# Kernel optimization log

Hardware: AMD Instinct MI355X
Metric: run time of the kernel (lower is better)

The kernel has to match this reference:

```python
import jax, jax.numpy as jnp
import numpy as np

H, C = 16, 5           # GAT heads, per-head out channels
SIZE = 500             # max_pool_x size (time bins)
GAT_SLOPE, ACT_SLOPE = 0.2, 0.01


def _lrelu(x, s):
    return jnp.where(x >= 0, x, s * x)


def _gat(x, src, dst, ea, mask, W, We, a_s, a_d, a_e, b):
    # PyG GATConv: shared src/dst lin, edge_dim, self-loops already appended by caller
    N = x.shape[0]
    xp = (x @ W.T).reshape(N, H, C)                                   # [N,H,C]
    al = (jnp.einsum('nhc,hc->nh', xp, a_s)[src]
          + jnp.einsum('nhc,hc->nh', xp, a_d)[dst]
          + jnp.einsum('ehc,hc->eh', (ea @ We.T).reshape(-1, H, C), a_e))  # [E,H]
    al = _lrelu(al, GAT_SLOPE)
    if mask is not None:  # masked-out edges contribute nothing (equivalent to edge removal)
        al = jnp.where(mask[:, None], al, -jnp.inf)
    m = jax.ops.segment_max(al, dst, num_segments=N)                  # finite: every node has a self-loop
    e = jnp.exp(al - m[dst])
    coef = e / jax.ops.segment_sum(e, dst, num_segments=N)[dst]       # segment softmax over incoming edges
    out = jax.ops.segment_sum(coef[:, :, None] * xp[src], dst, num_segments=N)
    return out.reshape(N, H * C) + b


def _conv(x, w, b):
    y = jax.lax.conv_general_dilated(x, w, (2,), [(1, 1)],
                                     dimension_numbers=('NCH', 'OIH', 'NCH'))
    return y + b[None, :, None]


def _mlp(z, w1, b1, w2, b2, w3, b3):
    z = _lrelu(z @ w1.T + b1, ACT_SLOPE)
    z = _lrelu(z @ w2.T + b2, ACT_SLOPE)
    return z @ w3.T + b3


def _forward(x, edge_attr,
             gat1_W, gat1_We, gat1_as, gat1_ad, gat1_ae, gat1_b,
             gat2_W, gat2_We, gat2_as, gat2_ad, gat2_ae, gat2_b,
             conv1_w, conv1_b, conv2_w, conv2_b, conv3_w, conv3_b,
             chi_w1, chi_b1, chi_w2, chi_b2, chi_w3, chi_b3,
             rp_w1, rp_b1, rp_w2, rp_b2, rp_w3, rp_b3,
             t0_w1, t0_b1, t0_w2, t0_b2, t0_w3, t0_b3,
             edge_index, num_graphs):
    N = x.shape[0]
    loops = jnp.arange(N, dtype=edge_index.dtype)
    src = jnp.concatenate([edge_index[0], loops])
    dst = jnp.concatenate([edge_index[1], loops])
    ea = jnp.concatenate([edge_attr, jnp.zeros((N, edge_attr.shape[1]), edge_attr.dtype)], axis=0)
    timing = x[:, 2].astype(jnp.int32)   # non-differentiable, like .to(torch.long)

    h = _gat(x, src, dst, ea, None, gat1_W, gat1_We, gat1_as, gat1_ad, gat1_ae, gat1_b)
    mask2 = jnp.concatenate([edge_attr[:, 0] > 1.0, jnp.ones((N,), bool)])  # EdgeV[:,0]>1 + self loops
    h = _gat(h, src, dst, ea, mask2, gat2_W, gat2_We, gat2_as, gat2_ad, gat2_ae, gat2_b)

    # max_pool_x(cluster=Timing, batch, size=500): scatter-max into B*500 slots,
    # empty slots -> 0 (torch_scatter semantics); then view(-1, 80, 500)
    pooled = jax.ops.segment_max(h, timing, num_segments=num_graphs * SIZE)
    pooled = jnp.where(jnp.isfinite(pooled), pooled, 0.0)
    z = pooled.reshape(num_graphs, H * C, SIZE)

    z = _lrelu(_conv(z, conv1_w, conv1_b), ACT_SLOPE)   # [B,16,247]
    z = _lrelu(_conv(z, conv2_w, conv2_b), ACT_SLOPE)   # [B,16,120]
    z = _lrelu(_conv(z, conv3_w, conv3_b), ACT_SLOPE)   # [B,16,57]
    L = z.shape[-1]
    nw = (L - 10) // 10 + 1                              # MaxPool1d(k=10,s=10) -> 5
    z = z[..., :nw * 10].reshape(z.shape[0], z.shape[1], nw, 10).max(-1)
    z = z.reshape(z.shape[0], -1)                        # [B,80]

    chi0 = jnp.tanh(_mlp(z, chi_w1, chi_b1, chi_w2, chi_b2, chi_w3, chi_b3))
    rp = _mlp(z, rp_w1, rp_b1, rp_w2, rp_b2, rp_w3, rp_b3)
    t0 = _mlp(z, t0_w1, t0_b1, t0_w2, t0_b2, t0_w3, t0_b3)
    return jnp.concatenate([chi0, rp, t0], axis=1)       # [B,3]


def setup_inputs() -> dict:
    key = jax.random.key(0)
    ki = iter(jax.random.split(key, 50))
    N, E, B = 100_000, 1_200_000, 64
    x = jax.random.normal(next(ki), (N, 5), jnp.float32)
    timing = jax.random.randint(next(ki), (N,), 0, SIZE)
    x = x.at[:, 2].set(timing.astype(jnp.float32))       # Timing column holds integer bins
    src = jax.random.randint(next(ki), (E,), 0, N, dtype=jnp.int32)
    off = jax.random.randint(next(ki), (E,), 1, N, dtype=jnp.int32)
    dst = (src + off) % N                                # no pre-existing self-loops (PyG strips them)
    edge_index = jnp.stack([src, dst])
    edge_attr = jax.random.uniform(next(ki), (E, 2), jnp.float32) * 3.0  # ~2/3 pass col0>1 mask
    batch = jnp.sort(jax.random.randint(next(ki), (N,), 0, B, dtype=jnp.int32))

    def p(shape, scale=0.1):
        return jax.random.normal(next(ki), shape, jnp.float32) * scale

    return dict(
        x=x, edge_attr=edge_attr,
        gat1_W=p((80, 5)), gat1_We=p((80, 2)), gat1_as=p((16, 5)), gat1_ad=p((16, 5)), gat1_ae=p((16, 5)), gat1_b=p((80,)),
        gat2_W=p((80, 80)), gat2_We=p((80, 2)), gat2_as=p((16, 5)), gat2_ad=p((16, 5)), gat2_ae=p((16, 5)), gat2_b=p((80,)),
        conv1_w=p((16, 80, 10)), conv1_b=p((16,)),
        conv2_w=p((16, 16, 10)), conv2_b=p((16,)),
        conv3_w=p((16, 16, 10)), conv3_b=p((16,)),
        chi_w1=p((128, 80)), chi_b1=p((128,)), chi_w2=p((128, 128)), chi_b2=p((128,)), chi_w3=p((1, 128)), chi_b3=p((1,)),
        rp_w1=p((128, 80)), rp_b1=p((128,)), rp_w2=p((128, 128)), rp_b2=p((128,)), rp_w3=p((1, 128)), rp_b3=p((1,)),
        t0_w1=p((128, 80)), t0_b1=p((128,)), t0_w2=p((128, 128)), t0_b2=p((128,)), t0_w3=p((1, 128)), t0_b3=p((1,)),
        edge_index=edge_index, batch=batch, num_graphs=B)


def reference(x, edge_attr,
              gat1_W, gat1_We, gat1_as, gat1_ad, gat1_ae, gat1_b,
              gat2_W, gat2_We, gat2_as, gat2_ad, gat2_ae, gat2_b,
              conv1_w, conv1_b, conv2_w, conv2_b, conv3_w, conv3_b,
              chi_w1, chi_b1, chi_w2, chi_b2, chi_w3, chi_b3,
              rp_w1, rp_b1, rp_w2, rp_b2, rp_w3, rp_b3,
              t0_w1, t0_b1, t0_w2, t0_b2, t0_w3, t0_b3,
              edge_index, batch, num_graphs):
    del batch  # only used in torch to compute batch_size (passed here as num_graphs)
    return _forward(x, edge_attr,
                    gat1_W, gat1_We, gat1_as, gat1_ad, gat1_ae, gat1_b,
                    gat2_W, gat2_We, gat2_as, gat2_ad, gat2_ae, gat2_b,
                    conv1_w, conv1_b, conv2_w, conv2_b, conv3_w, conv3_b,
                    chi_w1, chi_b1, chi_w2, chi_b2, chi_w3, chi_b3,
                    rp_w1, rp_b1, rp_w2, rp_b2, rp_w3, rp_b3,
                    t0_w1, t0_b1, t0_w2, t0_b2, t0_w3, t0_b3,
                    edge_index, num_graphs)
```

## Files before the change

kernel.cpp:

```cpp
#include <hip/hip_runtime.h>
#include <math.h>

#define DEV static __device__ __forceinline__

DEV unsigned fenc(float f) {
    unsigned u = __float_as_uint(f);
    return (u & 0x80000000u) ? ~u : (u | 0x80000000u);
}
DEV float fdec(unsigned u) {
    return __uint_as_float((u & 0x80000000u) ? (u ^ 0x80000000u) : ~u);
}
DEV void atomic_max_u32(unsigned* p, unsigned v) {
    __hip_atomic_fetch_max(p, v, __ATOMIC_RELAXED, __HIP_MEMORY_SCOPE_AGENT);
}
DEV unsigned bf16(float f) {
    unsigned u = __float_as_uint(f);
    return (u + 0x7FFFu + ((u >> 16) & 1u)) >> 16;
}
DEV float unbf16(unsigned s) { return __uint_as_float(s << 16); }

__global__ void k_proj5t(const float* __restrict__ x, const float* __restrict__ W,
                         const float* __restrict__ a_s, const float* __restrict__ a_d,
                         unsigned short* __restrict__ xpb, float* __restrict__ dterm, int N) {
    int i = blockIdx.x * blockDim.x + threadIdx.x;
    if (i >= N * 16) return;
    int n = i >> 4, h = i & 15;
    float xr[5];
    #pragma unroll
    for (int j = 0; j < 5; ++j) xr[j] = x[(size_t)n * 5 + j];
    float o[5];
    #pragma unroll
    for (int c = 0; c < 5; ++c) {
        const float* wr = W + (size_t)(h * 5 + c) * 5;
        float s = 0.f;
        #pragma unroll
        for (int j = 0; j < 5; ++j) s += xr[j] * wr[j];
        o[c] = s;
    }
    float ss = 0.f, sd = 0.f;
    #pragma unroll
    for (int c = 0; c < 5; ++c) { ss += o[c] * a_s[h * 5 + c]; sd += o[c] * a_d[h * 5 + c]; }
    unsigned* p = (unsigned*)(xpb + (size_t)n * 96 + h * 6);
    p[0] = bf16(o[0]) | (bf16(o[1]) << 16);
    p[1] = bf16(o[2]) | (bf16(o[3]) << 16);
    p[2] = bf16(o[4]) | (bf16(ss) << 16);
    dterm[i] = sd;
}

__global__ __launch_bounds__(256) void k_proj80t(
    const unsigned short* __restrict__ in,
    const float* __restrict__ W,
    const float* __restrict__ a_s, const float* __restrict__ a_d,
    unsigned short* __restrict__ xpb, float* __restrict__ dterm, int N) {
    __shared__ float XS[16 * 136];
    __shared__ float WS[16 * 81];
    int tid = threadIdx.x;
    int n0 = blockIdx.x * 128;
    int h = tid & 15, ng = tid >> 4;

    float acc[8][5];
    #pragma unroll
    for (int j = 0; j < 8; ++j)
        #pragma unroll
        for (int c = 0; c < 5; ++c) acc[j][c] = 0.f;

    for (int k0 = 0; k0 < 80; k0 += 16) {
        __syncthreads();
        {
            int r = tid >> 1;
            int halfk = (tid & 1) * 8;
            int n = n0 + r; if (n >= N) n = N - 1;
            const uint4 v = *(const uint4*)(in + (size_t)n * 80 + k0 + halfk);
            unsigned uu[4] = {v.x, v.y, v.z, v.w};
            #pragma unroll
            for (int j = 0; j < 4; ++j) {
                XS[(halfk + 2 * j)     * 136 + r] = unbf16(uu[j] & 0xffff);
                XS[(halfk + 2 * j + 1) * 136 + r] = unbf16(uu[j] >> 16);
            }
        }
        {
            #pragma unroll
            for (int i = 0; i < 5; ++i) {
                int j = tid + i * 256;
                int oc = j >> 4, kk = j & 15;
                WS[kk * 81 + oc] = W[(size_t)oc * 80 + k0 + kk];
            }
        }
        __syncthreads();
        #pragma unroll
        for (int kk = 0; kk < 16; ++kk) {
            float4 xa = *(const float4*)&XS[kk * 136 + ng * 8];
            float4 xb = *(const float4*)&XS[kk * 136 + ng * 8 + 4];
            float wv[5];
            #pragma unroll
            for (int c = 0; c < 5; ++c) wv[c] = WS[kk * 81 + h * 5 + c];
            float xv[8] = {xa.x, xa.y, xa.z, xa.w, xb.x, xb.y, xb.z, xb.w};
            #pragma unroll
            for (int j = 0; j < 8; ++j)
                #pragma unroll
                for (int c = 0; c < 5; ++c) acc[j][c] += xv[j] * wv[c];
        }
    }
    float as_[5], ad_[5];
    #pragma unroll
    for (int c = 0; c < 5; ++c) { as_[c] = a_s[h * 5 + c]; ad_[c] = a_d[h * 5 + c]; }
    #pragma unroll
    for (int j = 0; j < 8; ++j) {
        int n = n0 + ng * 8 + j;
        if (n < N) {
            float ss = 0.f, sd = 0.f;
            #pragma unroll
            for (int c = 0; c < 5; ++c) { ss += acc[j][c] * as_[c]; sd += acc[j][c] * ad_[c]; }
            unsigned* p = (unsigned*)(xpb + (size_t)n * 96 + h * 6);
            p[0] = bf16(acc[j][0]) | (bf16(acc[j][1]) << 16);
            p[1] = bf16(acc[j][2]) | (bf16(acc[j][3]) << 16);
            p[2] = bf16(acc[j][4]) | (bf16(ss) << 16);
            dterm[n * 16 + h] = sd;
        }
    }
}

__global__ void k_hist(const int* __restrict__ dst, int* __restrict__ deg, int E) {
    int e4 = (blockIdx.x * blockDim.x + threadIdx.x) * 4;
    if (e4 >= E) return;
    if (e4 + 3 < E) {
        int4 d = *(const int4*)(dst + e4);
        __hip_atomic_fetch_add(&deg[d.x], 1, __ATOMIC_RELAXED, __HIP_MEMORY_SCOPE_AGENT);
        __hip_atomic_fetch_add(&deg[d.y], 1, __ATOMIC_RELAXED, __HIP_MEMORY_SCOPE_AGENT);
        __hip_atomic_fetch_add(&deg[d.z], 1, __ATOMIC_RELAXED, __HIP_MEMORY_SCOPE_AGENT);
        __hip_atomic_fetch_add(&deg[d.w], 1, __ATOMIC_RELAXED, __HIP_MEMORY_SCOPE_AGENT);
    } else {
        for (int e = e4; e < E; ++e)
            __hip_atomic_fetch_add(&deg[dst[e]], 1, __ATOMIC_RELAXED, __HIP_MEMORY_SCOPE_AGENT);
    }
}

#define SCAN_B 256
__global__ void k_bsum(const int* __restrict__ deg, int* __restrict__ bsum, int N) {
    __shared__ int sm[SCAN_B];
    int i = blockIdx.x * SCAN_B + threadIdx.x;
    sm[threadIdx.x] = (i < N) ? deg[i] : 0;
    __syncthreads();
    for (int s = SCAN_B / 2; s > 0; s >>= 1) {
        if (threadIdx.x < s) sm[threadIdx.x] += sm[threadIdx.x + s];
        __syncthreads();
    }
    if (threadIdx.x == 0) bsum[blockIdx.x] = sm[0];
}

__global__ void k_bscan(int* __restrict__ bsum, int G) {
    __shared__ int sm[512];
    int t = threadIdx.x;
    int orig = (t < G) ? bsum[t] : 0;
    sm[t] = orig;
    __syncthreads();
    for (int s = 1; s < 512; s <<= 1) {
        int v = (t >= s) ? sm[t - s] : 0;
        __syncthreads();
        sm[t] += v;
        __syncthreads();
    }
    if (t < G) bsum[t] = sm[t] - orig;
}

__global__ void k_apply(const int* __restrict__ deg, int* __restrict__ off,
                        int* __restrict__ bcur, const int* __restrict__ bsum, int N) {
    __shared__ int sm[SCAN_B];
    int i = blockIdx.x * SCAN_B + threadIdx.x;
    int v = (i < N) ? deg[i] : 0;
    sm[threadIdx.x] = v;
    __syncthreads();
    for (int s = 1; s < SCAN_B; s <<= 1) {
        int t = (threadIdx.x >= s) ? sm[threadIdx.x - s] : 0;
        __syncthreads();
        sm[threadIdx.x] += t;
        __syncthreads();
    }
    if (i < N) {
        int excl = bsum[blockIdx.x] + sm[threadIdx.x] - v;
        off[i] = excl;
        if ((i & 255) == 0) bcur[i >> 8] = excl;
        if (i == N - 1) off[N] = excl + v;
    }
}

#define BIN_TILE 4096
__global__ __launch_bounds__(256) void k_bin(const int* __restrict__ src,
        const int* __restrict__ dst, const float* __restrict__ ea,
        int* __restrict__ bcur, uint4* __restrict__ ebuf, int E, int NB) {
    __shared__ int cnt[512];
    __shared__ int base[512];
    int tid = threadIdx.x;
    for (int b = tid; b < NB; b += 256) cnt[b] = 0;
    __syncthreads();
    int e0 = blockIdx.x * BIN_TILE;
    #pragma unroll
    for (int k = 0; k < BIN_TILE / 256; ++k) {
        int e = e0 + k * 256 + tid;
        if (e < E) atomicAdd(&cnt[((unsigned)dst[e]) >> 8], 1);
    }
    __syncthreads();
    for (int b = tid; b < NB; b += 256) {
        int c = cnt[b];
        base[b] = c ? __hip_atomic_fetch_add(&bcur[b], c, __ATOMIC_RELAXED,
                                             __HIP_MEMORY_SCOPE_AGENT) : 0;
        cnt[b] = 0;
    }
    __syncthreads();
    #pragma unroll
    for (int k = 0; k < BIN_TILE / 256; ++k) {
        int e = e0 + k * 256 + tid;
        if (e < E) {
            int d = dst[e];
            int b = ((unsigned)d) >> 8;
            int r = atomicAdd(&cnt[b], 1);
            float a0 = ea[2 * e], a1 = ea[2 * e + 1];
            unsigned s = (unsigned)src[e] | (a0 > 1.0f ? 0x80000000u : 0u);
            ebuf[base[b] + r] = make_uint4(s, bf16(a0) | (bf16(a1) << 16), (unsigned)d, 0u);
        }
    }
}

__global__ __launch_bounds__(256) void k_perm(const int* __restrict__ off,
        const uint4* __restrict__ ebuf, uint2* __restrict__ erec, int N) {
    __shared__ int cur[256];
    int b = blockIdx.x, tid = threadIdx.x;
    int d0 = b << 8;
    int dEnd = d0 + 256; if (dEnd > N) dEnd = N;
    if (d0 + tid < N) cur[tid] = off[d0 + tid];
    int seg0 = off[d0], seg1 = off[dEnd];
    __syncthreads();
    for (int i = seg0 + tid; i < seg1; i += 256) {
        uint4 r = ebuf[i];
        int p = atomicAdd(&cur[(int)r.z - d0], 1);
        erec[p] = make_uint2(r.x, r.y);
    }
}

template<bool MASKED, bool OUT_BF16>
__global__ void k_gat(const int* __restrict__ off, const uint2* __restrict__ erec,
                      const float* __restrict__ dterm,
                      const float* __restrict__ We, const float* __restrict__ a_e,
                      const unsigned short* __restrict__ xpb,
                      const float* __restrict__ bias, void* __restrict__ hout, int N) {
    int i = blockIdx.x * blockDim.x + threadIdx.x;
    if (i >= N * 16) return;
    int d = i >> 4, h = i & 15;
    float q0 = 0.f, q1 = 0.f;
    #pragma unroll
    for (int c = 0; c < 5; ++c) {
        float ae = a_e[h * 5 + c];
        q0 += We[(h * 5 + c) * 2 + 0] * ae;
        q1 += We[(h * 5 + c) * 2 + 1] * ae;
    }
    float dt = dterm[i];
    int e0 = off[d], e1 = off[d + 1];

    float m, den = 1.f, n0, n1, n2, n3, n4;
    {
        const uint3 v = *(const uint3*)(xpb + (size_t)d * 96 + h * 6);
        n0 = unbf16(v.x & 0xffff); n1 = unbf16(v.x >> 16);
        n2 = unbf16(v.y & 0xffff); n3 = unbf16(v.y >> 16);
        n4 = unbf16(v.z & 0xffff);
        float sl = unbf16(v.z >> 16) + dt;
        m = fmaxf(sl, 0.2f * sl);
    }

    uint2 r_cur = make_uint2(0, 0), r_nxt = make_uint2(0, 0);
    uint3 v_cur = make_uint3(0, 0, 0), v_nxt = make_uint3(0, 0, 0);
    if (e0 < e1) {
        r_cur = erec[e0];
        if (!MASKED || (r_cur.x >> 31))
            v_cur = *(const uint3*)(xpb + (size_t)(r_cur.x & 0x7fffffff) * 96 + h * 6);
    }
    if (e0 + 1 < e1) r_nxt = erec[e0 + 1];
    for (int e = e0; e < e1; ++e) {
        uint2 r_n2 = make_uint2(0, 0);
        if (e + 2 < e1) r_n2 = erec[e + 2];
        if (e + 1 < e1 && (!MASKED || (r_nxt.x >> 31)))
            v_nxt = *(const uint3*)(xpb + (size_t)(r_nxt.x & 0x7fffffff) * 96 + h * 6);
        bool keep = !MASKED || (r_cur.x >> 31);
        if (keep) {
            float ea0 = unbf16(r_cur.y & 0xffff), ea1 = unbf16(r_cur.y >> 16);
            uint3 v = v_cur;
            float st = unbf16(v.z >> 16);
            float al = st + dt + ea0 * q0 + ea1 * q1;
            al = fmaxf(al, 0.2f * al);
            float x0 = unbf16(v.x & 0xffff), x1 = unbf16(v.x >> 16);
            float x2 = unbf16(v.y & 0xffff), x3 = unbf16(v.y >> 16);
            float x4 = unbf16(v.z & 0xffff);
            bool gt = al > m;
            float t = __expf(-fabsf(al - m));
            float c = gt ? t : 1.f;
            float w = gt ? 1.f : t;
            m = fmaxf(m, al);
            den = den * c + w;
            n0 = n0 * c + w * x0;
            n1 = n1 * c + w * x1;
            n2 = n2 * c + w * x2;
            n3 = n3 * c + w * x3;
            n4 = n4 * c + w * x4;
        }
        r_cur = r_nxt; r_nxt = r_n2; v_cur = v_nxt;
    }
    float inv = 1.0f / den;
    const float* br = bias + h * 5;
    float v0 = n0 * inv + br[0];
    float v1 = n1 * inv + br[1];
    float v2 = n2 * inv + br[2];
    float v3 = n3 * inv + br[3];
    float v4 = n4 * inv + br[4];
    if (OUT_BF16) {
        unsigned short* orow = (unsigned short*)hout + (size_t)d * 80 + h * 5;
        orow[0] = (unsigned short)bf16(v0);
        orow[1] = (unsigned short)bf16(v1);
        orow[2] = (unsigned short)bf16(v2);
        orow[3] = (unsigned short)bf16(v3);
        orow[4] = (unsigned short)bf16(v4);
    } else {
        float* orow = (float*)hout + (size_t)d * 80 + h * 5;
        orow[0] = v0; orow[1] = v1; orow[2] = v2; orow[3] = v3; orow[4] = v4;
    }
}

__global__ void k_pool8(const float* __restrict__ x, const float* __restrict__ h2,
                        unsigned* __restrict__ psl, int N) {
    int i = blockIdx.x * blockDim.x + threadIdx.x;
    if (i >= N * 80) return;
    int n = i / 80, ch = i % 80;
    int t = (int)x[(size_t)n * 5 + 2];
    unsigned* slice = psl + (size_t)(blockIdx.x & 7) * 40000;
    atomic_max_u32(&slice[t * 80 + ch], fenc(h2[i]));
}

__global__ void k_poolred(const unsigned* __restrict__ psl, float* __restrict__ pool) {
    int i = blockIdx.x * blockDim.x + threadIdx.x;
    if (i >= 40000) return;
    unsigned m = 0u;
    #pragma unroll
    for (int s = 0; s < 8; ++s) m = max(m, psl[s * 40000 + i]);
    pool[i] = (m == 0u) ? 0.f : fdec(m);
}

__global__ __launch_bounds__(256) void k_conv1(const float* __restrict__ pool,
        const float* __restrict__ w, const float* __restrict__ b,
        float* __restrict__ c1) {
    __shared__ float XS[80 * 44];
    __shared__ float WS[16 * 972];
    int gg = blockIdx.x >> 4, chunk = blockIdx.x & 15;
    int t0 = chunk * 16;
    int tid = threadIdx.x;
    for (int idx = tid; idx < 80 * 44; idx += 256) {
        int ic = idx / 44, j = idx % 44;
        int p = 2 * t0 - 1 + j;
        XS[idx] = (gg == 0 && j < 41 && p >= 0 && p < 500) ? pool[ic * 500 + p] : 0.f;
    }
    for (int idx = tid; idx < 12800; idx += 256) {
        int oc = idx / 800, r = idx % 800;
        int ic = r / 10, k = r % 10;
        WS[oc * 972 + ic * 12 + k] = w[idx];
    }
    __syncthreads();
    int oc = tid >> 4, tg = tid & 15;
    float acc = 0.f;
    for (int ic = 0; ic < 80; ++ic) {
        const float* xr = &XS[ic * 44 + 2 * tg];
        const float* wr = &WS[oc * 972 + ic * 12];
        #pragma unroll
        for (int k = 0; k < 10; ++k) acc += xr[k] * wr[k];
    }
    int t = t0 + tg;
    if (t < 247) {
        float s = acc + b[oc];
        c1[(size_t)gg * 3952 + oc * 247 + t] = s >= 0.f ? s : 0.01f * s;
    }
}

__global__ __launch_bounds__(128) void k_conv2(const float* __restrict__ c1,
        const float* __restrict__ w2c, const float* __restrict__ b2c,
        float* __restrict__ c2g) {
    __shared__ float Z1[16 * 248];
    __shared__ float WS[160];
    int g = blockIdx.x >> 4, oc = blockIdx.x & 15;
    int tid = threadIdx.x;
    for (int idx = tid; idx < 16 * 247; idx += 128) {
        int ic = idx / 247, t = idx % 247;
        Z1[ic * 248 + t] = c1[(size_t)g * 3952 + idx];
    }
    for (int idx = tid; idx < 160; idx += 128) WS[idx] = w2c[oc * 160 + idx];
    __syncthreads();
    if (tid < 120) {
        float s = b2c[oc];
        #pragma unroll 4
        for (int ic = 0; ic < 16; ++ic) {
            const float* xr = &Z1[ic * 248];
            const float* wr = &WS[ic * 10];
            #pragma unroll
            for (int k = 0; k < 10; ++k) {
                int p = 2 * tid + k - 1;
                if (p >= 0 && p < 247) s += xr[p] * wr[k];
            }
        }
        c2g[g * 1920 + oc * 120 + tid] = s >= 0.f ? s : 0.01f * s;
    }
}

__global__ __launch_bounds__(128) void k_conv3(const float* __restrict__ c2g,
        const float* __restrict__ w3c, const float* __restrict__ b3c,
        float* __restrict__ c3g) {
    __shared__ float Z2[16 * 121];
    __shared__ float WS[160];
    int g = blockIdx.x >> 4, oc = blockIdx.x & 15;
    int tid = threadIdx.x;
    for (int idx = tid; idx < 16 * 120; idx += 128) {
        int ic = idx / 120, t = idx % 120;
        Z2[ic * 121 + t] = c2g[g * 1920 + idx];
    }
    for (int idx = tid; idx < 160; idx += 128) WS[idx] = w3c[oc * 160 + idx];
    __syncthreads();
    if (tid < 57) {
        float s = b3c[oc];
        #pragma unroll 4
        for (int ic = 0; ic < 16; ++ic) {
            const float* xr = &Z2[ic * 121];
            const float* wr = &WS[ic * 10];
            #pragma unroll
            for (int k = 0; k < 10; ++k) {
                int p = 2 * tid + k - 1;
                if (p >= 0 && p < 120) s += xr[p] * wr[k];
            }
        }
        c3g[g * 912 + oc * 57 + tid] = s >= 0.f ? s : 0.01f * s;
    }
}

struct HeadW { const float *w1, *b1, *w2, *b2, *w3, *b3; };

__global__ __launch_bounds__(128) void k_heads(const float* __restrict__ c3g,
        HeadW hw0, HeadW hw1, HeadW hw2, float* __restrict__ houts) {
    __shared__ float Z3[16 * 57];
    __shared__ float ZF[80], HB[128], HC[128];
    __shared__ float partial[2];
    int g = blockIdx.x / 3, hd = blockIdx.x % 3;
    int tid = threadIdx.x;
    const HeadW hw = (hd == 0) ? hw0 : (hd == 1) ? hw1 : hw2;
    for (int idx = tid; idx < 912; idx += 128) Z3[idx] = c3g[g * 912 + idx];
    __syncthreads();
    if (tid < 80) {
        int ch = tid / 5, wd = tid % 5;
        const float* p = &Z3[ch * 57 + wd * 10];
        float m = p[0];
        #pragma unroll
        for (int k = 1; k < 10; ++k) m = fmaxf(m, p[k]);
        ZF[tid] = m;
    }
    __syncthreads();
    float s = hw.b1[tid];
    for (int k = 0; k < 80; ++k) s += ZF[k] * hw.w1[tid * 80 + k];
    HB[tid] = s >= 0.f ? s : 0.01f * s;
    __syncthreads();
    s = hw.b2[tid];
    for (int k = 0; k < 128; ++k) s += HB[k] * hw.w2[tid * 128 + k];
    HC[tid] = s >= 0.f ? s : 0.01f * s;
    __syncthreads();
    float p = HC[tid] * hw.w3[tid];
    #pragma unroll
    for (int o = 32; o > 0; o >>= 1) p += __shfl_down(p, o, 64);
    if ((tid & 63) == 0) partial[tid >> 6] = p;
    __syncthreads();
    if (tid == 0) {
        float o = partial[0] + partial[1] + hw.b3[0];
        houts[g * 3 + hd] = (hd == 0) ? tanhf(o) : o;
    }
}

__global__ void k_bcast(const float* __restrict__ houts, float* __restrict__ out, int B3) {
    int i = blockIdx.x * blockDim.x + threadIdx.x;
    if (i >= B3) return;
    out[i] = (i < 3) ? houts[i] : houts[3 + (i % 3)];
}

extern "C" void kernel_launch(void* const* d_in, const int* in_sizes, int n_in,
                              void* d_out, int out_size, void* d_ws, size_t ws_size,
                              hipStream_t stream) {
    const float* x     = (const float*)d_in[0];
    const float* ea    = (const float*)d_in[1];
    const float* g1_W  = (const float*)d_in[2];
    const float* g1_We = (const float*)d_in[3];
    const float* g1_as = (const float*)d_in[4];
    const float* g1_ad = (const float*)d_in[5];
    const float* g1_ae = (const float*)d_in[6];
    const float* g1_b  = (const float*)d_in[7];
    const float* g2_W  = (const float*)d_in[8];
    const float* g2_We = (const float*)d_in[9];
    const float* g2_as = (const float*)d_in[10];
    const float* g2_ad = (const float*)d_in[11];
    const float* g2_ae = (const float*)d_in[12];
    const float* g2_b  = (const float*)d_in[13];
    const float* c1w = (const float*)d_in[14]; const float* c1b = (const float*)d_in[15];
    const float* c2w = (const float*)d_in[16]; const float* c2b = (const float*)d_in[17];
    const float* c3w = (const float*)d_in[18]; const float* c3b = (const float*)d_in[19];
    const int*   eidx = (const int*)d_in[38];
    float* out = (float*)d_out;

    const int N = in_sizes[0] / 5;
    const int E = in_sizes[38] / 2;
    const int B = out_size / 3;
    const int* src = eidx;
    const int* dst = eidx + E;

    float* ws = (float*)d_ws;
    size_t o = 0;
    auto alloc = [&](size_t n) { float* p = ws + o; o = (o + n + 3) & ~(size_t)3; return p; };
    unsigned short* xpb = (unsigned short*)alloc((size_t)N * 48);
    float*    Hbuf  = alloc((size_t)N * 80);
    float*    dterm = alloc((size_t)N * 16);
    int*      off   = (int*)alloc((size_t)N + 1);
    int*      cur   = (int*)alloc((size_t)N);
    int*      bsum  = (int*)alloc(512);
    int*      bcur  = (int*)alloc(512);
    uint4*    ebuf  = (uint4*)alloc((size_t)E * 4);
    uint2*    erec  = (uint2*)alloc((size_t)E * 2);
    unsigned* psl   = (unsigned*)alloc(8 * 40000);
    float*    pool  = alloc(40000);
    float*    c1    = alloc(2 * 3952);
    float*    c2g   = alloc(2 * 1920);
    float*    c3g   = alloc(2 * 912);
    float*    houts = alloc(8);

    const int BS = 256;
    auto blocks = [&](long long n) { return (int)((n + BS - 1) / BS); };
    const int G = (N + SCAN_B - 1) / SCAN_B;
    const int NB = (N + 255) / 256;

    hipMemsetAsync(cur, 0, (size_t)N * 4, stream);
    hipMemsetAsync(psl, 0, 8 * 40000 * 4, stream);
    k_hist<<<blocks((E + 3) / 4), BS, 0, stream>>>(dst, cur, E);
    k_bsum<<<G, SCAN_B, 0, stream>>>(cur, bsum, N);
    k_bscan<<<1, 512, 0, stream>>>(bsum, G);
    k_apply<<<G, SCAN_B, 0, stream>>>(cur, off, bcur, bsum, N);
    k_bin<<<(E + BIN_TILE - 1) / BIN_TILE, 256, 0, stream>>>(src, dst, ea, bcur, ebuf, E, NB);
    k_perm<<<NB, 256, 0, stream>>>(off, ebuf, erec, N);

    k_proj5t<<<blocks((long long)N * 16), BS, 0, stream>>>(x, g1_W, g1_as, g1_ad,
                                                           xpb, dterm, N);
    k_gat<false, true><<<blocks((long long)N * 16), BS, 0, stream>>>(
        off, erec, dterm, g1_We, g1_ae, xpb, g1_b, (void*)Hbuf, N);

    k_proj80t<<<(N + 127) / 128, 256, 0, stream>>>((const unsigned short*)Hbuf, g2_W,
                                                   g2_as, g2_ad, xpb, dterm, N);
    k_gat<true, false><<<blocks((long long)N * 16), BS, 0, stream>>>(
        off, erec, dterm, g2_We, g2_ae, xpb, g2_b, (void*)Hbuf, N);

    k_pool8<<<blocks((long long)N * 80), BS, 0, stream>>>(x, Hbuf, psl, N);
    k_poolred<<<blocks(40000), BS, 0, stream>>>(psl, pool);

    k_conv1<<<32, 256, 0, stream>>>(pool, c1w, c1b, c1);
    k_conv2<<<32, 128, 0, stream>>>(c1, c2w, c2b, c2g);
    k_conv3<<<32, 128, 0, stream>>>(c2g, c3w, c3b, c3g);
    HeadW h0 = {(const float*)d_in[20], (const float*)d_in[21], (const float*)d_in[22],
                (const float*)d_in[23], (const float*)d_in[24], (const float*)d_in[25]};
    HeadW h1 = {(const float*)d_in[26], (const float*)d_in[27], (const float*)d_in[28],
                (const float*)d_in[29], (const float*)d_in[30], (const float*)d_in[31]};
    HeadW h2 = {(const float*)d_in[32], (const float*)d_in[33], (const float*)d_in[34],
                (const float*)d_in[35], (const float*)d_in[36], (const float*)d_in[37]};
    k_heads<<<6, 128, 0, stream>>>(c3g, h0, h1, h2, houts);
    k_bcast<<<blocks(B * 3), BS, 0, stream>>>(houts, out, B * 3);
}
```

Measured before the change: 451.9 us.

## Replace atomic max pooling with time-bin CSR gather and fuse head broadcast

Max-pool over time bins now builds a CSR of nodes per time bin (histogram, scan, scatter) and gathers bf16 GAT2 outputs per bin with a plain max. This replaces per-element atomic max into eight slices and the reduction kernel. GAT2 now writes bf16 output to halve traffic. The head-broadcast kernel is folded into k_heads. The GAT inner loop uses float2 packed math, and bf16 unpacking uses a mask in place of a shift. The cost is three extra small kernels, plus a scatter order that is nondeterministic but harmless for max. Pooling now sees bf16-rounded values.

```diff
diff --git a/kernel.cpp b/kernel.cpp
--- a/kernel.cpp
+++ b/kernel.cpp
@@ -3,21 +3,17 @@
 
 #define DEV static __device__ __forceinline__
 
-DEV unsigned fenc(float f) {
-    unsigned u = __float_as_uint(f);
-    return (u & 0x80000000u) ? ~u : (u | 0x80000000u);
-}
-DEV float fdec(unsigned u) {
-    return __uint_as_float((u & 0x80000000u) ? (u ^ 0x80000000u) : ~u);
-}
-DEV void atomic_max_u32(unsigned* p, unsigned v) {
-    __hip_atomic_fetch_max(p, v, __ATOMIC_RELAXED, __HIP_MEMORY_SCOPE_AGENT);
-}
 DEV unsigned bf16(float f) {
     unsigned u = __float_as_uint(f);
     return (u + 0x7FFFu + ((u >> 16) & 1u)) >> 16;
 }
 DEV float unbf16(unsigned s) { return __uint_as_float(s << 16); }
+DEV float blo(unsigned u) { return __uint_as_float(u << 16); }
+DEV float bhi(unsigned u) { return __uint_as_float(u & 0xffff0000u); }
+DEV float2 pkmul(float2 a, float2 b) { return make_float2(a.x * b.x, a.y * b.y); }
+DEV float2 pkfma(float2 a, float2 b, float2 c) {
+    return make_float2(fmaf(a.x, b.x, c.x), fmaf(a.y, b.y, c.y));
+}
 
 __global__ void k_proj5t(const float* __restrict__ x, const float* __restrict__ W,
                          const float* __restrict__ a_s, const float* __restrict__ a_d,
@@ -74,8 +70,8 @@
             unsigned uu[4] = {v.x, v.y, v.z, v.w};
             #pragma unroll
             for (int j = 0; j < 4; ++j) {
-                XS[(halfk + 2 * j)     * 136 + r] = unbf16(uu[j] & 0xffff);
-                XS[(halfk + 2 * j + 1) * 136 + r] = unbf16(uu[j] >> 16);
+                XS[(halfk + 2 * j)     * 136 + r] = blo(uu[j]);
+                XS[(halfk + 2 * j + 1) * 136 + r] = bhi(uu[j]);
             }
         }
         {
@@ -256,13 +252,14 @@
     float dt = dterm[i];
     int e0 = off[d], e1 = off[d + 1];
 
-    float m, den = 1.f, n0, n1, n2, n3, n4;
+    float m, den = 1.f, n4;
+    float2 n01, n23;
     {
         const uint3 v = *(const uint3*)(xpb + (size_t)d * 96 + h * 6);
-        n0 = unbf16(v.x & 0xffff); n1 = unbf16(v.x >> 16);
-        n2 = unbf16(v.y & 0xffff); n3 = unbf16(v.y >> 16);
-        n4 = unbf16(v.z & 0xffff);
-        float sl = unbf16(v.z >> 16) + dt;
+        n01 = make_float2(blo(v.x), bhi(v.x));
+        n23 = make_float2(blo(v.y), bhi(v.y));
+        n4 = blo(v.z);
+        float sl = bhi(v.z) + dt;
         m = fmaxf(sl, 0.2f * sl);
     }
 
@@ -281,34 +278,29 @@
             v_nxt = *(const uint3*)(xpb + (size_t)(r_nxt.x & 0x7fffffff) * 96 + h * 6);
         bool keep = !MASKED || (r_cur.x >> 31);
         if (keep) {
-            float ea0 = unbf16(r_cur.y & 0xffff), ea1 = unbf16(r_cur.y >> 16);
+            float ea0 = blo(r_cur.y), ea1 = bhi(r_cur.y);
             uint3 v = v_cur;
-            float st = unbf16(v.z >> 16);
-            float al = st + dt + ea0 * q0 + ea1 * q1;
+            float al = bhi(v.z) + dt + ea0 * q0 + ea1 * q1;
             al = fmaxf(al, 0.2f * al);
-            float x0 = unbf16(v.x & 0xffff), x1 = unbf16(v.x >> 16);
-            float x2 = unbf16(v.y & 0xffff), x3 = unbf16(v.y >> 16);
-            float x4 = unbf16(v.z & 0xffff);
             bool gt = al > m;
             float t = __expf(-fabsf(al - m));
             float c = gt ? t : 1.f;
             float w = gt ? 1.f : t;
             m = fmaxf(m, al);
-            den = den * c + w;
-            n0 = n0 * c + w * x0;
-            n1 = n1 * c + w * x1;
-            n2 = n2 * c + w * x2;
-            n3 = n3 * c + w * x3;
-            n4 = n4 * c + w * x4;
+            float2 c2 = make_float2(c, c), w2 = make_float2(w, w);
+            den = fmaf(den, c, w);
+            n01 = pkfma(n01, c2, pkmul(w2, make_float2(blo(v.x), bhi(v.x))));
+            n23 = pkfma(n23, c2, pkmul(w2, make_float2(blo(v.y), bhi(v.y))));
+            n4  = fmaf(n4, c, w * blo(v.z));
         }
         r_cur = r_nxt; r_nxt = r_n2; v_cur = v_nxt;
     }
     float inv = 1.0f / den;
     const float* br = bias + h * 5;
-    float v0 = n0 * inv + br[0];
-    float v1 = n1 * inv + br[1];
-    float v2 = n2 * inv + br[2];
-    float v3 = n3 * inv + br[3];
+    float v0 = n01.x * inv + br[0];
+    float v1 = n01.y * inv + br[1];
+    float v2 = n23.x * inv + br[2];
+    float v3 = n23.y * inv + br[3];
     float v4 = n4 * inv + br[4];
     if (OUT_BF16) {
         unsigned short* orow = (unsigned short*)hout + (size_t)d * 80 + h * 5;
@@ -323,23 +315,52 @@
     }
 }
 
-__global__ void k_pool8(const float* __restrict__ x, const float* __restrict__ h2,
-                        unsigned* __restrict__ psl, int N) {
-    int i = blockIdx.x * blockDim.x + threadIdx.x;
-    if (i >= N * 80) return;
-    int n = i / 80, ch = i % 80;
+__global__ void k_thist(const float* __restrict__ x, int* __restrict__ t500, int N) {
+    int n = blockIdx.x * blockDim.x + threadIdx.x;
+    if (n >= N) return;
     int t = (int)x[(size_t)n * 5 + 2];
-    unsigned* slice = psl + (size_t)(blockIdx.x & 7) * 40000;
-    atomic_max_u32(&slice[t * 80 + ch], fenc(h2[i]));
-}
-
-__global__ void k_poolred(const unsigned* __restrict__ psl, float* __restrict__ pool) {
-    int i = blockIdx.x * blockDim.x + threadIdx.x;
-    if (i >= 40000) return;
-    unsigned m = 0u;
-    #pragma unroll
-    for (int s = 0; s < 8; ++s) m = max(m, psl[s * 40000 + i]);
-    pool[i] = (m == 0u) ? 0.f : fdec(m);
+    __hip_atomic_fetch_add(&t500[t], 1, __ATOMIC_RELAXED, __HIP_MEMORY_SCOPE_AGENT);
+}
+
+__global__ void k_tscan(const int* __restrict__ t500, int* __restrict__ toff,
+                        int* __restrict__ tcur) {
+    __shared__ int sm[512];
+    int t = threadIdx.x;
+    int v = (t < 500) ? t500[t] : 0;
+    sm[t] = v;
+    __syncthreads();
+    for (int s = 1; s < 512; s <<= 1) {
+        int u = (t >= s) ? sm[t - s] : 0;
+        __syncthreads();
+        sm[t] += u;
+        __syncthreads();
+    }
+    if (t < 500) { int excl = sm[t] - v; toff[t] = excl; tcur[t] = excl; }
+    if (t == 511) toff[500] = sm[511];
+}
+
+__global__ void k_tscat(const float* __restrict__ x, int* __restrict__ tcur,
+                        int* __restrict__ tidx, int N) {
+    int n = blockIdx.x * blockDim.x + threadIdx.x;
+    if (n >= N) return;
+    int t = (int)x[(size_t)n * 5 + 2];
+    int p = __hip_atomic_fetch_add(&tcur[t], 1, __ATOMIC_RELAXED, __HIP_MEMORY_SCOPE_AGENT);
+    tidx[p] = n;
+}
+
+__global__ __launch_bounds__(128) void k_poolmax(const int* __restrict__ toff,
+        const int* __restrict__ tidx, const unsigned short* __restrict__ h2b,
+        float* __restrict__ pool) {
+    int t = blockIdx.x, ch = threadIdx.x;
+    int e0 = toff[t], e1 = toff[t + 1];
+    float m = -INFINITY;
+    int n_nxt = (e0 < e1) ? tidx[e0] : 0;
+    for (int e = e0; e < e1; ++e) {
+        int n = n_nxt;
+        if (e + 1 < e1) n_nxt = tidx[e + 1];
+        if (ch < 80) m = fmaxf(m, unbf16(h2b[(size_t)n * 80 + ch]));
+    }
+    if (ch < 80) pool[t * 80 + ch] = (e0 == e1) ? 0.f : m;
 }
 
 __global__ __launch_bounds__(256) void k_conv1(const float* __restrict__ pool,
@@ -437,10 +458,11 @@
 struct HeadW { const float *w1, *b1, *w2, *b2, *w3, *b3; };
 
 __global__ __launch_bounds__(128) void k_heads(const float* __restrict__ c3g,
-        HeadW hw0, HeadW hw1, HeadW hw2, float* __restrict__ houts) {
+        HeadW hw0, HeadW hw1, HeadW hw2, float* __restrict__ out, int B) {
     __shared__ float Z3[16 * 57];
     __shared__ float ZF[80], HB[128], HC[128];
     __shared__ float partial[2];
+    __shared__ float oval;
     int g = blockIdx.x / 3, hd = blockIdx.x % 3;
     int tid = threadIdx.x;
     const HeadW hw = (hd == 0) ? hw0 : (hd == 1) ? hw1 : hw2;
@@ -470,14 +492,15 @@
     __syncthreads();
     if (tid == 0) {
         float o = partial[0] + partial[1] + hw.b3[0];
-        houts[g * 3 + hd] = (hd == 0) ? tanhf(o) : o;
-    }
-}
-
-__global__ void k_bcast(const float* __restrict__ houts, float* __restrict__ out, int B3) {
-    int i = blockIdx.x * blockDim.x + threadIdx.x;
-    if (i >= B3) return;
-    out[i] = (i < 3) ? houts[i] : houts[3 + (i % 3)];
+        o = (hd == 0) ? tanhf(o) : o;
+        oval = o;
+        if (g == 0) out[hd] = o;
+    }
+    __syncthreads();
+    if (g == 1) {
+        float o = oval;
+        for (int gg = 1 + tid; gg < B; gg += 128) out[gg * 3 + hd] = o;
+    }
 }
 
 extern "C" void kernel_launch(void* const* d_in, const int* in_sizes, int n_in,
@@ -521,12 +544,14 @@
     int*      bcur  = (int*)alloc(512);
     uint4*    ebuf  = (uint4*)alloc((size_t)E * 4);
     uint2*    erec  = (uint2*)alloc((size_t)E * 2);
-    unsigned* psl   = (unsigned*)alloc(8 * 40000);
+    int*      t500  = (int*)alloc(512);
+    int*      toff  = (int*)alloc(512);
+    int*      tcur  = (int*)alloc(512);
+    int*      tidx  = (int*)alloc((size_t)N);
     float*    pool  = alloc(40000);
     float*    c1    = alloc(2 * 3952);
     float*    c2g   = alloc(2 * 1920);
     float*    c3g   = alloc(2 * 912);
-    float*    houts = alloc(8);
 
     const int BS = 256;
     auto blocks = [&](long long n) { return (int)((n + BS - 1) / BS); };
@@ -534,13 +559,16 @@
     const int NB = (N + 255) / 256;
 
     hipMemsetAsync(cur, 0, (size_t)N * 4, stream);
-    hipMemsetAsync(psl, 0, 8 * 40000 * 4, stream);
+    hipMemsetAsync(t500, 0, 512 * 4, stream);
     k_hist<<<blocks((E + 3) / 4), BS, 0, stream>>>(dst, cur, E);
     k_bsum<<<G, SCAN_B, 0, stream>>>(cur, bsum, N);
     k_bscan<<<1, 512, 0, stream>>>(bsum, G);
     k_apply<<<G, SCAN_B, 0, stream>>>(cur, off, bcur, bsum, N);
     k_bin<<<(E + BIN_TILE - 1) / BIN_TILE, 256, 0, stream>>>(src, dst, ea, bcur, ebuf, E, NB);
     k_perm<<<NB, 256, 0, stream>>>(off, ebuf, erec, N);
+    k_thist<<<blocks(N), BS, 0, stream>>>(x, t500, N);
+    k_tscan<<<1, 512, 0, stream>>>(t500, toff, tcur);
+    k_tscat<<<blocks(N), BS, 0, stream>>>(x, tcur, tidx, N);
 
     k_proj5t<<<blocks((long long)N * 16), BS, 0, stream>>>(x, g1_W, g1_as, g1_ad,
                                                            xpb, dterm, N);
@@ -549,11 +577,10 @@
 
     k_proj80t<<<(N + 127) / 128, 256, 0, stream>>>((const unsigned short*)Hbuf, g2_W,
                                                    g2_as, g2_ad, xpb, dterm, N);
-    k_gat<true, false><<<blocks((long long)N * 16), BS, 0, stream>>>(
+    k_gat<true, true><<<blocks((long long)N * 16), BS, 0, stream>>>(
         off, erec, dterm, g2_We, g2_ae, xpb, g2_b, (void*)Hbuf, N);
 
-    k_pool8<<<blocks((long long)N * 80), BS, 0, stream>>>(x, Hbuf, psl, N);
-    k_poolred<<<blocks(40000), BS, 0, stream>>>(psl, pool);
+    k_poolmax<<<500, 128, 0, stream>>>(toff, tidx, (const unsigned short*)Hbuf, pool);
 
     k_conv1<<<32, 256, 0, stream>>>(pool, c1w, c1b, c1);
     k_conv2<<<32, 128, 0, stream>>>(c1, c2w, c2b, c2g);
@@ -564,6 +591,5 @@
                 (const float*)d_in[29], (const float*)d_in[30], (const float*)d_in[31]};
     HeadW h2 = {(const float*)d_in[32], (const float*)d_in[33], (const float*)d_in[34],
                 (const float*)d_in[35], (const float*)d_in[36], (const float*)d_in[37]};
-    k_heads<<<6, 128, 0, stream>>>(c3g, h0, h1, h2, houts);
-    k_bcast<<<blocks(B * 3), BS, 0, stream>>>(houts, out, B * 3);
-}
+    k_heads<<<6, 128, 0, stream>>>(c3g, h0, h1, h2, out, B);
+}
```

Measured after the change: 557.4 us. +23.4%, slower.

## Build CSR via bucket counts, write GAT2 output as bf16, fuse broadcast into heads

Applied to the files above, without the earlier changes.

Drops the per-node atomic degree histogram and the three-kernel global scan. Edges are now counted per 256-node bucket in shared memory, those bucket counts are scanned, and per-node offsets are computed inside the permutation kernel with a local block scan. The second GAT layer writes bf16 output so pooling reads half the bytes, and the broadcast kernel is merged into the heads kernel. The pooled max now operates on bf16-rounded values, which costs some precision.

```diff
diff --git a/kernel.cpp b/kernel.cpp
--- a/kernel.cpp
+++ b/kernel.cpp
@@ -120,71 +120,46 @@
     }
 }
 
-__global__ void k_hist(const int* __restrict__ dst, int* __restrict__ deg, int E) {
-    int e4 = (blockIdx.x * blockDim.x + threadIdx.x) * 4;
-    if (e4 >= E) return;
-    if (e4 + 3 < E) {
-        int4 d = *(const int4*)(dst + e4);
-        __hip_atomic_fetch_add(&deg[d.x], 1, __ATOMIC_RELAXED, __HIP_MEMORY_SCOPE_AGENT);
-        __hip_atomic_fetch_add(&deg[d.y], 1, __ATOMIC_RELAXED, __HIP_MEMORY_SCOPE_AGENT);
-        __hip_atomic_fetch_add(&deg[d.z], 1, __ATOMIC_RELAXED, __HIP_MEMORY_SCOPE_AGENT);
-        __hip_atomic_fetch_add(&deg[d.w], 1, __ATOMIC_RELAXED, __HIP_MEMORY_SCOPE_AGENT);
-    } else {
-        for (int e = e4; e < E; ++e)
-            __hip_atomic_fetch_add(&deg[dst[e]], 1, __ATOMIC_RELAXED, __HIP_MEMORY_SCOPE_AGENT);
-    }
-}
-
-#define SCAN_B 256
-__global__ void k_bsum(const int* __restrict__ deg, int* __restrict__ bsum, int N) {
-    __shared__ int sm[SCAN_B];
-    int i = blockIdx.x * SCAN_B + threadIdx.x;
-    sm[threadIdx.x] = (i < N) ? deg[i] : 0;
-    __syncthreads();
-    for (int s = SCAN_B / 2; s > 0; s >>= 1) {
-        if (threadIdx.x < s) sm[threadIdx.x] += sm[threadIdx.x + s];
-        __syncthreads();
-    }
-    if (threadIdx.x == 0) bsum[blockIdx.x] = sm[0];
-}
-
-__global__ void k_bscan(int* __restrict__ bsum, int G) {
+#define BIN_TILE 4096
+__global__ __launch_bounds__(256) void k_cnt512(const int* __restrict__ dst,
+        int* __restrict__ bcnt, int E, int NB) {
+    __shared__ int cnt[512];
+    int tid = threadIdx.x;
+    for (int b = tid; b < NB; b += 256) cnt[b] = 0;
+    __syncthreads();
+    int e0 = blockIdx.x * BIN_TILE;
+    #pragma unroll
+    for (int k = 0; k < BIN_TILE / 256; ++k) {
+        int e = e0 + k * 256 + tid;
+        if (e < E) atomicAdd(&cnt[((unsigned)dst[e]) >> 8], 1);
+    }
+    __syncthreads();
+    for (int b = tid; b < NB; b += 256) {
+        int c = cnt[b];
+        if (c) __hip_atomic_fetch_add(&bcnt[b], c, __ATOMIC_RELAXED, __HIP_MEMORY_SCOPE_AGENT);
+    }
+}
+
+__global__ void k_scan512(const int* __restrict__ bcnt, int* __restrict__ boff,
+                          int* __restrict__ bcur, int* __restrict__ off,
+                          int NB, int N, int E) {
     __shared__ int sm[512];
     int t = threadIdx.x;
-    int orig = (t < G) ? bsum[t] : 0;
-    sm[t] = orig;
+    int v = (t < NB) ? bcnt[t] : 0;
+    sm[t] = v;
     __syncthreads();
     for (int s = 1; s < 512; s <<= 1) {
-        int v = (t >= s) ? sm[t - s] : 0;
+        int u = (t >= s) ? sm[t - s] : 0;
         __syncthreads();
-        sm[t] += v;
+        sm[t] += u;
         __syncthreads();
     }
-    if (t < G) bsum[t] = sm[t] - orig;
-}
-
-__global__ void k_apply(const int* __restrict__ deg, int* __restrict__ off,
-                        int* __restrict__ bcur, const int* __restrict__ bsum, int N) {
-    __shared__ int sm[SCAN_B];
-    int i = blockIdx.x * SCAN_B + threadIdx.x;
-    int v = (i < N) ? deg[i] : 0;
-    sm[threadIdx.x] = v;
-    __syncthreads();
-    for (int s = 1; s < SCAN_B; s <<= 1) {
-        int t = (threadIdx.x >= s) ? sm[threadIdx.x - s] : 0;
-        __syncthreads();
-        sm[threadIdx.x] += t;
-        __syncthreads();
-    }
-    if (i < N) {
-        int excl = bsum[blockIdx.x] + sm[threadIdx.x] - v;
-        off[i] = excl;
-        if ((i & 255) == 0) bcur[i >> 8] = excl;
-        if (i == N - 1) off[N] = excl + v;
-    }
-}
-
-#define BIN_TILE 4096
+    int excl = sm[t] - v;
+    if (t < NB) { boff[t] = excl; bcur[t] = excl; }
+    if (t == NB - 1) boff[NB] = excl + v;
+    if (t == 0) off[N] = E;
+}
+
 __global__ __launch_bounds__(256) void k_bin(const int* __restrict__ src,
         const int* __restrict__ dst, const float* __restrict__ ea,
         int* __restrict__ bcur, uint4* __restrict__ ebuf, int E, int NB) {
@@ -221,18 +196,35 @@
     }
 }
 
-__global__ __launch_bounds__(256) void k_perm(const int* __restrict__ off,
-        const uint4* __restrict__ ebuf, uint2* __restrict__ erec, int N) {
-    __shared__ int cur[256];
+__global__ __launch_bounds__(256) void k_perm2(const int* __restrict__ boff,
+        const uint4* __restrict__ ebuf, uint2* __restrict__ erec,
+        int* __restrict__ off, int N) {
+    __shared__ int cnt[256];
+    __shared__ int sm[256];
     int b = blockIdx.x, tid = threadIdx.x;
     int d0 = b << 8;
-    int dEnd = d0 + 256; if (dEnd > N) dEnd = N;
-    if (d0 + tid < N) cur[tid] = off[d0 + tid];
-    int seg0 = off[d0], seg1 = off[dEnd];
-    __syncthreads();
-    for (int i = seg0 + tid; i < seg1; i += 256) {
+    int s0 = boff[b], s1 = boff[b + 1];
+    cnt[tid] = 0;
+    __syncthreads();
+    for (int i = s0 + tid; i < s1; i += 256)
+        atomicAdd(&cnt[(int)ebuf[i].z - d0], 1);
+    __syncthreads();
+    int v = cnt[tid];
+    sm[tid] = v;
+    __syncthreads();
+    for (int s = 1; s < 256; s <<= 1) {
+        int u = (tid >= s) ? sm[tid - s] : 0;
+        __syncthreads();
+        sm[tid] += u;
+        __syncthreads();
+    }
+    int excl = sm[tid] - v;
+    if (d0 + tid < N) off[d0 + tid] = s0 + excl;
+    cnt[tid] = s0 + excl;
+    __syncthreads();
+    for (int i = s0 + tid; i < s1; i += 256) {
         uint4 r = ebuf[i];
-        int p = atomicAdd(&cur[(int)r.z - d0], 1);
+        int p = atomicAdd(&cnt[(int)r.z - d0], 1);
         erec[p] = make_uint2(r.x, r.y);
     }
 }
@@ -323,14 +315,14 @@
     }
 }
 
-__global__ void k_pool8(const float* __restrict__ x, const float* __restrict__ h2,
+__global__ void k_pool8(const float* __restrict__ x, const unsigned short* __restrict__ h2b,
                         unsigned* __restrict__ psl, int N) {
     int i = blockIdx.x * blockDim.x + threadIdx.x;
     if (i >= N * 80) return;
     int n = i / 80, ch = i % 80;
     int t = (int)x[(size_t)n * 5 + 2];
     unsigned* slice = psl + (size_t)(blockIdx.x & 7) * 40000;
-    atomic_max_u32(&slice[t * 80 + ch], fenc(h2[i]));
+    atomic_max_u32(&slice[t * 80 + ch], fenc(unbf16(h2b[i])));
 }
 
 __global__ void k_poolred(const unsigned* __restrict__ psl, float* __restrict__ pool) {
@@ -437,10 +429,11 @@
 struct HeadW { const float *w1, *b1, *w2, *b2, *w3, *b3; };
 
 __global__ __launch_bounds__(128) void k_heads(const float* __restrict__ c3g,
-        HeadW hw0, HeadW hw1, HeadW hw2, float* __restrict__ houts) {
+        HeadW hw0, HeadW hw1, HeadW hw2, float* __restrict__ out, int B) {
     __shared__ float Z3[16 * 57];
     __shared__ float ZF[80], HB[128], HC[128];
     __shared__ float partial[2];
+    __shared__ float oval;
     int g = blockIdx.x / 3, hd = blockIdx.x % 3;
     int tid = threadIdx.x;
     const HeadW hw = (hd == 0) ? hw0 : (hd == 1) ? hw1 : hw2;
@@ -470,14 +463,15 @@
     __syncthreads();
     if (tid == 0) {
         float o = partial[0] + partial[1] + hw.b3[0];
-        houts[g * 3 + hd] = (hd == 0) ? tanhf(o) : o;
-    }
-}
-
-__global__ void k_bcast(const float* __restrict__ houts, float* __restrict__ out, int B3) {
-    int i = blockIdx.x * blockDim.x + threadIdx.x;
-    if (i >= B3) return;
-    out[i] = (i < 3) ? houts[i] : houts[3 + (i % 3)];
+        o = (hd == 0) ? tanhf(o) : o;
+        oval = o;
+        if (g == 0) out[hd] = o;
+    }
+    __syncthreads();
+    if (g == 1) {
+        float o = oval;
+        for (int gg = 1 + tid; gg < B; gg += 128) out[gg * 3 + hd] = o;
+    }
 }
 
 extern "C" void kernel_launch(void* const* d_in, const int* in_sizes, int n_in,
@@ -516,8 +510,8 @@
     float*    Hbuf  = alloc((size_t)N * 80);
     float*    dterm = alloc((size_t)N * 16);
     int*      off   = (int*)alloc((size_t)N + 1);
-    int*      cur   = (int*)alloc((size_t)N);
-    int*      bsum  = (int*)alloc(512);
+    int*      bcnt  = (int*)alloc(512);
+    int*      boff  = (int*)alloc(516);
     int*      bcur  = (int*)alloc(512);
     uint4*    ebuf  = (uint4*)alloc((size_t)E * 4);
     uint2*    erec  = (uint2*)alloc((size_t)E * 2);
@@ -526,21 +520,18 @@
     float*    c1    = alloc(2 * 3952);
     float*    c2g   = alloc(2 * 1920);
     float*    c3g   = alloc(2 * 912);
-    float*    houts = alloc(8);
 
     const int BS = 256;
     auto blocks = [&](long long n) { return (int)((n + BS - 1) / BS); };
-    const int G = (N + SCAN_B - 1) / SCAN_B;
     const int NB = (N + 255) / 256;
-
-    hipMemsetAsync(cur, 0, (size_t)N * 4, stream);
+    const int TILES = (E + BIN_TILE - 1) / BIN_TILE;
+
+    hipMemsetAsync(bcnt, 0, 512 * 4, stream);
     hipMemsetAsync(psl, 0, 8 * 40000 * 4, stream);
-    k_hist<<<blocks((E + 3) / 4), BS, 0, stream>>>(dst, cur, E);
-    k_bsum<<<G, SCAN_B, 0, stream>>>(cur, bsum, N);
-    k_bscan<<<1, 512, 0, stream>>>(bsum, G);
-    k_apply<<<G, SCAN_B, 0, stream>>>(cur, off, bcur, bsum, N);
-    k_bin<<<(E + BIN_TILE - 1) / BIN_TILE, 256, 0, stream>>>(src, dst, ea, bcur, ebuf, E, NB);
-    k_perm<<<NB, 256, 0, stream>>>(off, ebuf, erec, N);
+    k_cnt512<<<TILES, 256, 0, stream>>>(dst, bcnt, E, NB);
+    k_scan512<<<1, 512, 0, stream>>>(bcnt, boff, bcur, off, NB, N, E);
+    k_bin<<<TILES, 256, 0, stream>>>(src, dst, ea, bcur, ebuf, E, NB);
+    k_perm2<<<NB, 256, 0, stream>>>(boff, ebuf, erec, off, N);
 
     k_proj5t<<<blocks((long long)N * 16), BS, 0, stream>>>(x, g1_W, g1_as, g1_ad,
                                                            xpb, dterm, N);
@@ -549,10 +540,11 @@
 
     k_proj80t<<<(N + 127) / 128, 256, 0, stream>>>((const unsigned short*)Hbuf, g2_W,
                                                    g2_as, g2_ad, xpb, dterm, N);
-    k_gat<true, false><<<blocks((long long)N * 16), BS, 0, stream>>>(
+    k_gat<true, true><<<blocks((long long)N * 16), BS, 0, stream>>>(
         off, erec, dterm, g2_We, g2_ae, xpb, g2_b, (void*)Hbuf, N);
 
-    k_pool8<<<blocks((long long)N * 80), BS, 0, stream>>>(x, Hbuf, psl, N);
+    k_pool8<<<blocks((long long)N * 80), BS, 0, stream>>>(x, (const unsigned short*)Hbuf,
+                                                          psl, N);
     k_poolred<<<blocks(40000), BS, 0, stream>>>(psl, pool);
 
     k_conv1<<<32, 256, 0, stream>>>(pool, c1w, c1b, c1);
@@ -564,6 +556,5 @@
                 (const float*)d_in[29], (const float*)d_in[30], (const float*)d_in[31]};
     HeadW h2 = {(const float*)d_in[32], (const float*)d_in[33], (const float*)d_in[34],
                 (const float*)d_in[35], (const float*)d_in[36], (const float*)d_in[37]};
-    k_heads<<<6, 128, 0, stream>>>(c3g, h0, h1, h2, houts);
-    k_bcast<<<blocks(B * 3), BS, 0, stream>>>(houts, out, B * 3);
-}
+    k_heads<<<6, 128, 0, stream>>>(c3g, h0, h1, h2, out, B);
+}
```

New measurement: 416.2 us. 7.9% less time.
